# Kernel optimization log

Hardware: AMD Instinct MI355X
Metric: run time of the kernel (lower is better)

The kernel has to match this reference:

```python
import jax, jax.numpy as jnp
import numpy as np

H = 64  # hidden_size

def _lstm_layer(x, Wih, Whh, bih, bhh):
    # x: [B,T,I]; Wih: [4H,I]; Whh: [4H,H]; biases: [4H]
    # PyTorch gate order: i, f, g, o
    xg = jnp.einsum('bti,gi->btg', x, Wih) + (bih + bhh)  # [B,T,4H]
    B = x.shape[0]
    h0 = jnp.zeros((B, H), x.dtype)
    c0 = jnp.zeros((B, H), x.dtype)

    def step(carry, xg_t):
        h, c = carry
        gates = xg_t + h @ Whh.T  # [B,4H]
        i, f, g, o = jnp.split(gates, 4, axis=-1)
        i = jax.nn.sigmoid(i)
        f = jax.nn.sigmoid(f)
        g = jnp.tanh(g)
        o = jax.nn.sigmoid(o)
        c = f * c + i * g
        h = o * jnp.tanh(c)
        return (h, c), h

    _, hs = jax.lax.scan(step, (h0, c0), jnp.swapaxes(xg, 0, 1))  # hs: [T,B,H]
    return jnp.swapaxes(hs, 0, 1)  # [B,T,H]


def setup_inputs() -> dict:
    key = jax.random.key(0)
    ks = jax.random.split(key, 13)
    B, T, I = 1024, 512, 32
    s = 0.1
    return {
        'x': jax.random.normal(ks[0], (B, T, I), jnp.float32),
        'Wih0': jax.random.normal(ks[1], (4 * H, I), jnp.float32) * s,
        'Whh0': jax.random.normal(ks[2], (4 * H, H), jnp.float32) * s,
        'bih0': jax.random.normal(ks[3], (4 * H,), jnp.float32) * s,
        'bhh0': jax.random.normal(ks[4], (4 * H,), jnp.float32) * s,
        'Wih1': jax.random.normal(ks[5], (4 * H, H), jnp.float32) * s,
        'Whh1': jax.random.normal(ks[6], (4 * H, H), jnp.float32) * s,
        'bih1': jax.random.normal(ks[7], (4 * H,), jnp.float32) * s,
        'bhh1': jax.random.normal(ks[8], (4 * H,), jnp.float32) * s,
        'fc1_w': jax.random.normal(ks[9], (32, H), jnp.float32) * s,
        'fc1_b': jax.random.normal(ks[10], (32,), jnp.float32) * s,
        'fc2_w': jax.random.normal(ks[11], (2, 32), jnp.float32) * s,
        'fc2_b': jax.random.normal(ks[12], (2,), jnp.float32) * s,
    }


def reference(x, Wih0, Whh0, bih0, bhh0, Wih1, Whh1, bih1, bhh1, fc1_w, fc1_b, fc2_w, fc2_b):
    # Inference mode: dropout layers are identity.
    h1 = _lstm_layer(x, Wih0, Whh0, bih0, bhh0)   # [B,T,H]
    h2 = _lstm_layer(h1, Wih1, Whh1, bih1, bhh1)  # [B,T,H]
    h = h2[:, -1, :]                               # [B,H]
    z = jax.nn.relu(h @ fc1_w.T + fc1_b)           # [B,32]
    return z @ fc2_w.T + fc2_b                     # [B,2]
```

## Files before the change

### kernel.cpp

```cpp
#include <hip/hip_runtime.h>
#include <math.h>

#define TLEN 512
#define NB   1024
#define HSTR 80
#define HLAY (4 * HSTR)
#define XCH  64
#define XBSTR (XCH * 32 + 16)
#define XHALF (4 * XBSTR)

#define NLOG2E  (-1.44269504f)
#define N2LOG2E (-2.88539008f)

typedef _Float16 f16;
typedef f16   f16x4 __attribute__((ext_vector_type(4)));
typedef f16   f16x8 __attribute__((ext_vector_type(8)));
typedef float f32x4 __attribute__((ext_vector_type(4)));

__device__ __forceinline__ float ex2(float x) {
#if __has_builtin(__builtin_amdgcn_exp2f)
    return __builtin_amdgcn_exp2f(x);
#else
    return exp2f(x);
#endif
}
__device__ __forceinline__ float rcp_(float x) { return __builtin_amdgcn_rcpf(x); }
__device__ __forceinline__ float sel4(f32x4 v, int g) {
    float a = (g & 1) ? v[1] : v[0];
    float b = (g & 1) ? v[3] : v[2];
    return (g & 2) ? b : a;
}

__global__ __launch_bounds__(512, 2) void lstm_fused(
    const float* __restrict__ x,
    const float* __restrict__ Wih0, const float* __restrict__ Whh0,
    const float* __restrict__ bih0, const float* __restrict__ bhh0,
    const float* __restrict__ Wih1, const float* __restrict__ Whh1,
    const float* __restrict__ bih1, const float* __restrict__ bhh1,
    const float* __restrict__ fc1w, const float* __restrict__ fc1b,
    const float* __restrict__ fc2w, const float* __restrict__ fc2b,
    float* __restrict__ out)
{
    __shared__ __align__(16) f16 x_lds[2 * XHALF];
    __shared__ __align__(16) f16 h1buf[2 * HLAY];
    __shared__ __align__(16) f16 h2buf[2 * HLAY];
    __shared__ float zbuf[4][33];

    const int tid   = threadIdx.x;
    const int lane  = tid & 63;
    const int w     = tid >> 6;
    const int wg    = w & 3;
    const bool isL0 = (w < 4);
    const int bc    = lane & 15;
    const int lq    = lane >> 4;
    const int G     = bc >> 2;
    const int b_own = bc & 3;
    const int bg0   = blockIdx.x * 4;

    const float wsc[4] = {NLOG2E, NLOG2E, N2LOG2E, NLOG2E};
    f16x8 A[4][4];
    f32x4 cb[4];
    #pragma unroll
    for (int g = 0; g < 4; ++g) {
        const int gr = g * 64 + 16 * wg + bc;
        #pragma unroll
        for (int s = 0; s < 4; ++s) {
            #pragma unroll
            for (int i = 0; i < 8; ++i) {
                int k = 32 * s + lq * 8 + i;
                float v = 0.0f;
                if (isL0) {
                    if (s < 3) v = (k < 32) ? Wih0[gr * 32 + k] : Whh0[gr * 64 + (k - 32)];
                } else {
                    v = (k < 64) ? Wih1[gr * 64 + k] : Whh1[gr * 64 + (k - 64)];
                }
                A[g][s][i] = (f16)(v * wsc[g]);
            }
        }
        #pragma unroll
        for (int r = 0; r < 4; ++r) {
            const int gd = g * 64 + 16 * wg + 4 * lq + r;
            float bb = isL0 ? (bih0[gd] + bhh0[gd]) : (bih1[gd] + bhh1[gd]);
            cb[g][r] = bb * wsc[g];
        }
    }

    for (int i = tid; i < 2 * HLAY; i += 512) { h1buf[i] = (f16)0; h2buf[i] = (f16)0; }

    const int rf_b   = tid >> 7;
    const int rf_rem = tid & 127;
#define REFILL(ch)                                                            \
    {                                                                         \
        f16* dst = x_lds + ((ch) & 1) * XHALF + rf_b * XBSTR;                 \
        const float4* src = (const float4*)(x +                               \
            ((long)(bg0 + rf_b) * TLEN + (ch) * XCH) * 32);                   \
        float4 v0 = src[rf_rem];                                              \
        float4 v1 = src[rf_rem + 128];                                        \
        float4 v2 = src[rf_rem + 256];                                        \
        float4 v3 = src[rf_rem + 384];                                        \
        f16x4 h;                                                              \
        h[0]=(f16)v0.x; h[1]=(f16)v0.y; h[2]=(f16)v0.z; h[3]=(f16)v0.w;       \
        *(f16x4*)(dst + (rf_rem)       * 4) = h;                              \
        h[0]=(f16)v1.x; h[1]=(f16)v1.y; h[2]=(f16)v1.z; h[3]=(f16)v1.w;       \
        *(f16x4*)(dst + (rf_rem + 128) * 4) = h;                              \
        h[0]=(f16)v2.x; h[1]=(f16)v2.y; h[2]=(f16)v2.z; h[3]=(f16)v2.w;       \
        *(f16x4*)(dst + (rf_rem + 256) * 4) = h;                              \
        h[0]=(f16)v3.x; h[1]=(f16)v3.y; h[2]=(f16)v3.z; h[3]=(f16)v3.w;       \
        *(f16x4*)(dst + (rf_rem + 384) * 4) = h;                              \
    }

    REFILL(0)
    __syncthreads();

    const int bch = b_own * HSTR + lq * 8;
    const int bxx = b_own * XBSTR + lq * 8;
    const int hwr = b_own * HSTR + 16 * wg + 4 * lq + G;

    float cst = 0.0f;

#define CELL_UPDATE(HBUF, PW)                                                 \
    {                                                                         \
        float pi = sel4(a0, G);                                               \
        float pf = sel4(a1, G);                                               \
        float pg = sel4(a2, G);                                               \
        float po = sel4(a3, G);                                               \
        float iv = rcp_(1.0f + ex2(pi));                                      \
        float fv = rcp_(1.0f + ex2(pf));                                      \
        float gv = fmaf(2.0f, rcp_(1.0f + ex2(pg)), -1.0f);                   \
        float ov = rcp_(1.0f + ex2(po));                                      \
        cst = fmaf(fv, cst, iv * gv);                                         \
        float tc = fmaf(2.0f, rcp_(1.0f + ex2(cst * N2LOG2E)), -1.0f);        \
        HBUF[(PW) * HLAY + hwr] = (f16)(ov * tc);                             \
    }

#define L0_PHASE(p, itv)                                                      \
    {                                                                         \
        f16x8 b0 = *(const f16x8*)(x_lds + (((itv) >> 6) & 1) * XHALF +       \
                                   ((itv) & (XCH - 1)) * 32 + bxx);           \
        f16x8 b1 = *(const f16x8*)(h1buf + ((p)^1) * HLAY + bch);             \
        f16x8 b2 = *(const f16x8*)(h1buf + ((p)^1) * HLAY + bch + 32);        \
        __builtin_amdgcn_s_setprio(1);                                        \
        f32x4 a0 = __builtin_amdgcn_mfma_f32_16x16x32_f16(A[0][0], b0, cb[0], 0,0,0); \
        f32x4 a1 = __builtin_amdgcn_mfma_f32_16x16x32_f16(A[1][0], b0, cb[1], 0,0,0); \
        f32x4 a2 = __builtin_amdgcn_mfma_f32_16x16x32_f16(A[2][0], b0, cb[2], 0,0,0); \
        f32x4 a3 = __builtin_amdgcn_mfma_f32_16x16x32_f16(A[3][0], b0, cb[3], 0,0,0); \
        a0 = __builtin_amdgcn_mfma_f32_16x16x32_f16(A[0][1], b1, a0, 0,0,0);  \
        a1 = __builtin_amdgcn_mfma_f32_16x16x32_f16(A[1][1], b1, a1, 0,0,0);  \
        a2 = __builtin_amdgcn_mfma_f32_16x16x32_f16(A[2][1], b1, a2, 0,0,0);  \
        a3 = __builtin_amdgcn_mfma_f32_16x16x32_f16(A[3][1], b1, a3, 0,0,0);  \
        a0 = __builtin_amdgcn_mfma_f32_16x16x32_f16(A[0][2], b2, a0, 0,0,0);  \
        a1 = __builtin_amdgcn_mfma_f32_16x16x32_f16(A[1][2], b2, a1, 0,0,0);  \
        a2 = __builtin_amdgcn_mfma_f32_16x16x32_f16(A[2][2], b2, a2, 0,0,0);  \
        a3 = __builtin_amdgcn_mfma_f32_16x16x32_f16(A[3][2], b2, a3, 0,0,0);  \
        __builtin_amdgcn_s_setprio(0);                                        \
        CELL_UPDATE(h1buf, p)                                                 \
    }

#define L1_PHASE(p)                                                           \
    {                                                                         \
        f16x8 b0 = *(const f16x8*)(h1buf + ((p)^1) * HLAY + bch);             \
        f16x8 b1 = *(const f16x8*)(h1buf + ((p)^1) * HLAY + bch + 32);        \
        f16x8 b2 = *(const f16x8*)(h2buf + (p) * HLAY + bch);                 \
        f16x8 b3 = *(const f16x8*)(h2buf + (p) * HLAY + bch + 32);            \
        __builtin_amdgcn_s_setprio(1);                                        \
        f32x4 a0 = __builtin_amdgcn_mfma_f32_16x16x32_f16(A[0][0], b0, cb[0], 0,0,0); \
        f32x4 a1 = __builtin_amdgcn_mfma_f32_16x16x32_f16(A[1][0], b0, cb[1], 0,0,0); \
        f32x4 a2 = __builtin_amdgcn_mfma_f32_16x16x32_f16(A[2][0], b0, cb[2], 0,0,0); \
        f32x4 a3 = __builtin_amdgcn_mfma_f32_16x16x32_f16(A[3][0], b0, cb[3], 0,0,0); \
        a0 = __builtin_amdgcn_mfma_f32_16x16x32_f16(A[0][1], b1, a0, 0,0,0);  \
        a1 = __builtin_amdgcn_mfma_f32_16x16x32_f16(A[1][1], b1, a1, 0,0,0);  \
        a2 = __builtin_amdgcn_mfma_f32_16x16x32_f16(A[2][1], b1, a2, 0,0,0);  \
        a3 = __builtin_amdgcn_mfma_f32_16x16x32_f16(A[3][1], b1, a3, 0,0,0);  \
        a0 = __builtin_amdgcn_mfma_f32_16x16x32_f16(A[0][2], b2, a0, 0,0,0);  \
        a1 = __builtin_amdgcn_mfma_f32_16x16x32_f16(A[1][2], b2, a1, 0,0,0);  \
        a2 = __builtin_amdgcn_mfma_f32_16x16x32_f16(A[2][2], b2, a2, 0,0,0);  \
        a3 = __builtin_amdgcn_mfma_f32_16x16x32_f16(A[3][2], b2, a3, 0,0,0);  \
        a0 = __builtin_amdgcn_mfma_f32_16x16x32_f16(A[0][3], b3, a0, 0,0,0);  \
        a1 = __builtin_amdgcn_mfma_f32_16x16x32_f16(A[1][3], b3, a1, 0,0,0);  \
        a2 = __builtin_amdgcn_mfma_f32_16x16x32_f16(A[2][3], b3, a2, 0,0,0);  \
        a3 = __builtin_amdgcn_mfma_f32_16x16x32_f16(A[3][3], b3, a3, 0,0,0);  \
        __builtin_amdgcn_s_setprio(0);                                        \
        CELL_UPDATE(h2buf, (p)^1)                                             \
    }

    if (isL0) L0_PHASE(0, 0)
    REFILL(1)
    __syncthreads();

    #pragma unroll 1
    for (int k = 0; k < 255; ++k) {
        if (isL0) L0_PHASE(1, 2 * k + 1) else L1_PHASE(1)
        __syncthreads();
        const int it2 = 2 * k + 2;
        if (isL0) L0_PHASE(0, it2) else L1_PHASE(0)
        if ((it2 & (XCH - 1)) == 0 && it2 <= TLEN - 2 * XCH)
            REFILL((it2 >> 6) + 1)
        __syncthreads();
    }

    if (isL0) L0_PHASE(1, 511) else L1_PHASE(1)
    __syncthreads();
    if (!isL0) L1_PHASE(0)
    __syncthreads();

#undef L0_PHASE
#undef L1_PHASE
#undef CELL_UPDATE
#undef REFILL

    const f16* h2f = h2buf + HLAY;
    if (tid < 128) {
        int b = tid >> 5, m = tid & 31;
        float z = fc1b[m];
        #pragma unroll
        for (int j = 0; j < 64; ++j)
            z = fmaf(fc1w[m * 64 + j], (float)h2f[b * HSTR + j], z);
        zbuf[b][m] = fmaxf(z, 0.0f);
    }
    __syncthreads();
    if (tid < 8) {
        int b = tid >> 1, o = tid & 1;
        float s = fc2b[o];
        #pragma unroll
        for (int m = 0; m < 32; ++m)
            s = fmaf(fc2w[o * 32 + m], zbuf[b][m], s);
        out[(long)(bg0 + b) * 2 + o] = s;
    }
}

extern "C" void kernel_launch(void* const* d_in, const int* in_sizes, int n_in,
                              void* d_out, int out_size, void* d_ws, size_t ws_size,
                              hipStream_t stream) {
    const float* x    = (const float*)d_in[0];
    const float* Wih0 = (const float*)d_in[1];
    const float* Whh0 = (const float*)d_in[2];
    const float* bih0 = (const float*)d_in[3];
    const float* bhh0 = (const float*)d_in[4];
    const float* Wih1 = (const float*)d_in[5];
    const float* Whh1 = (const float*)d_in[6];
    const float* bih1 = (const float*)d_in[7];
    const float* bhh1 = (const float*)d_in[8];
    const float* fc1w = (const float*)d_in[9];
    const float* fc1b = (const float*)d_in[10];
    const float* fc2w = (const float*)d_in[11];
    const float* fc2b = (const float*)d_in[12];
    float* out = (float*)d_out;

    lstm_fused<<<dim3(NB / 4), dim3(512), 0, stream>>>(
        x, Wih0, Whh0, bih0, bhh0, Wih1, Whh1, bih1, bhh1,
        fc1w, fc1b, fc2w, fc2b, out);
}
```

Measured before the change: 227.4 us.

## Split LSTM steps into MFMA and activation halves staggered between layers

```diff
diff --git a/kernel.cpp b/kernel.cpp
--- a/kernel.cpp
+++ b/kernel.cpp
@@ -31,7 +31,7 @@
     return (g & 2) ? b : a;
 }
 
-__global__ __launch_bounds__(512, 2) void lstm_fused(
+__global__ __launch_bounds__(512, 1) void lstm_fused(
     const float* __restrict__ x,
     const float* __restrict__ Wih0, const float* __restrict__ Whh0,
     const float* __restrict__ bih0, const float* __restrict__ bhh0,
@@ -89,27 +89,34 @@
 
     const int rf_b   = tid >> 7;
     const int rf_rem = tid & 127;
-#define REFILL(ch)                                                            \
+#define REFILL512(ch)                                                         \
     {                                                                         \
         f16* dst = x_lds + ((ch) & 1) * XHALF + rf_b * XBSTR;                 \
         const float4* src = (const float4*)(x +                               \
             ((long)(bg0 + rf_b) * TLEN + (ch) * XCH) * 32);                   \
-        float4 v0 = src[rf_rem];                                              \
-        float4 v1 = src[rf_rem + 128];                                        \
-        float4 v2 = src[rf_rem + 256];                                        \
-        float4 v3 = src[rf_rem + 384];                                        \
-        f16x4 h;                                                              \
-        h[0]=(f16)v0.x; h[1]=(f16)v0.y; h[2]=(f16)v0.z; h[3]=(f16)v0.w;       \
-        *(f16x4*)(dst + (rf_rem)       * 4) = h;                              \
-        h[0]=(f16)v1.x; h[1]=(f16)v1.y; h[2]=(f16)v1.z; h[3]=(f16)v1.w;       \
-        *(f16x4*)(dst + (rf_rem + 128) * 4) = h;                              \
-        h[0]=(f16)v2.x; h[1]=(f16)v2.y; h[2]=(f16)v2.z; h[3]=(f16)v2.w;       \
-        *(f16x4*)(dst + (rf_rem + 256) * 4) = h;                              \
-        h[0]=(f16)v3.x; h[1]=(f16)v3.y; h[2]=(f16)v3.z; h[3]=(f16)v3.w;       \
-        *(f16x4*)(dst + (rf_rem + 384) * 4) = h;                              \
-    }
-
-    REFILL(0)
+        _Pragma("unroll")                                                     \
+        for (int j = 0; j < 4; ++j) {                                         \
+            float4 v = src[rf_rem + 128 * j];                                 \
+            f16x4 hv;                                                         \
+            hv[0]=(f16)v.x; hv[1]=(f16)v.y; hv[2]=(f16)v.z; hv[3]=(f16)v.w;   \
+            *(f16x4*)(dst + (rf_rem + 128 * j) * 4) = hv;                     \
+        }                                                                     \
+    }
+#define REFILL256(ch)                                                         \
+    {                                                                         \
+        f16* dst = x_lds + ((ch) & 1) * XHALF + wg * XBSTR;                   \
+        const float4* src = (const float4*)(x +                               \
+            ((long)(bg0 + wg) * TLEN + (ch) * XCH) * 32);                     \
+        _Pragma("unroll")                                                     \
+        for (int j = 0; j < 8; ++j) {                                         \
+            float4 v = src[lane + 64 * j];                                    \
+            f16x4 hv;                                                         \
+            hv[0]=(f16)v.x; hv[1]=(f16)v.y; hv[2]=(f16)v.z; hv[3]=(f16)v.w;   \
+            *(f16x4*)(dst + (lane + 64 * j) * 4) = hv;                        \
+        }                                                                     \
+    }
+
+    REFILL512(0)
     __syncthreads();
 
     const int bch = b_own * HSTR + lq * 8;
@@ -117,33 +124,19 @@
     const int hwr = b_own * HSTR + 16 * wg + 4 * lq + G;
 
     float cst = 0.0f;
-
-#define CELL_UPDATE(HBUF, PW)                                                 \
-    {                                                                         \
-        float pi = sel4(a0, G);                                               \
-        float pf = sel4(a1, G);                                               \
-        float pg = sel4(a2, G);                                               \
-        float po = sel4(a3, G);                                               \
-        float iv = rcp_(1.0f + ex2(pi));                                      \
-        float fv = rcp_(1.0f + ex2(pf));                                      \
-        float gv = fmaf(2.0f, rcp_(1.0f + ex2(pg)), -1.0f);                   \
-        float ov = rcp_(1.0f + ex2(po));                                      \
-        cst = fmaf(fv, cst, iv * gv);                                         \
-        float tc = fmaf(2.0f, rcp_(1.0f + ex2(cst * N2LOG2E)), -1.0f);        \
-        HBUF[(PW) * HLAY + hwr] = (f16)(ov * tc);                             \
-    }
-
-#define L0_PHASE(p, itv)                                                      \
+    f32x4 a0 = {0.f,0.f,0.f,0.f}, a1 = a0, a2 = a0, a3 = a0;
+
+#define L0_MFMA(P, itv)                                                       \
     {                                                                         \
         f16x8 b0 = *(const f16x8*)(x_lds + (((itv) >> 6) & 1) * XHALF +       \
-                                   ((itv) & (XCH - 1)) * 32 + bxx);           \
-        f16x8 b1 = *(const f16x8*)(h1buf + ((p)^1) * HLAY + bch);             \
-        f16x8 b2 = *(const f16x8*)(h1buf + ((p)^1) * HLAY + bch + 32);        \
+                                   ((itv) & 63) * 32 + bxx);                  \
+        f16x8 b1 = *(const f16x8*)(h1buf + ((P)^1) * HLAY + bch);             \
+        f16x8 b2 = *(const f16x8*)(h1buf + ((P)^1) * HLAY + bch + 32);        \
         __builtin_amdgcn_s_setprio(1);                                        \
-        f32x4 a0 = __builtin_amdgcn_mfma_f32_16x16x32_f16(A[0][0], b0, cb[0], 0,0,0); \
-        f32x4 a1 = __builtin_amdgcn_mfma_f32_16x16x32_f16(A[1][0], b0, cb[1], 0,0,0); \
-        f32x4 a2 = __builtin_amdgcn_mfma_f32_16x16x32_f16(A[2][0], b0, cb[2], 0,0,0); \
-        f32x4 a3 = __builtin_amdgcn_mfma_f32_16x16x32_f16(A[3][0], b0, cb[3], 0,0,0); \
+        a0 = __builtin_amdgcn_mfma_f32_16x16x32_f16(A[0][0], b0, cb[0], 0,0,0); \
+        a1 = __builtin_amdgcn_mfma_f32_16x16x32_f16(A[1][0], b0, cb[1], 0,0,0); \
+        a2 = __builtin_amdgcn_mfma_f32_16x16x32_f16(A[2][0], b0, cb[2], 0,0,0); \
+        a3 = __builtin_amdgcn_mfma_f32_16x16x32_f16(A[3][0], b0, cb[3], 0,0,0); \
         a0 = __builtin_amdgcn_mfma_f32_16x16x32_f16(A[0][1], b1, a0, 0,0,0);  \
         a1 = __builtin_amdgcn_mfma_f32_16x16x32_f16(A[1][1], b1, a1, 0,0,0);  \
         a2 = __builtin_amdgcn_mfma_f32_16x16x32_f16(A[2][1], b1, a2, 0,0,0);  \
@@ -153,20 +146,19 @@
         a2 = __builtin_amdgcn_mfma_f32_16x16x32_f16(A[2][2], b2, a2, 0,0,0);  \
         a3 = __builtin_amdgcn_mfma_f32_16x16x32_f16(A[3][2], b2, a3, 0,0,0);  \
         __builtin_amdgcn_s_setprio(0);                                        \
-        CELL_UPDATE(h1buf, p)                                                 \
-    }
-
-#define L1_PHASE(p)                                                           \
-    {                                                                         \
-        f16x8 b0 = *(const f16x8*)(h1buf + ((p)^1) * HLAY + bch);             \
-        f16x8 b1 = *(const f16x8*)(h1buf + ((p)^1) * HLAY + bch + 32);        \
-        f16x8 b2 = *(const f16x8*)(h2buf + (p) * HLAY + bch);                 \
-        f16x8 b3 = *(const f16x8*)(h2buf + (p) * HLAY + bch + 32);            \
+    }
+
+#define L1_MFMA(P)                                                            \
+    {                                                                         \
+        f16x8 b0 = *(const f16x8*)(h1buf + ((P)^1) * HLAY + bch);             \
+        f16x8 b1 = *(const f16x8*)(h1buf + ((P)^1) * HLAY + bch + 32);        \
+        f16x8 b2 = *(const f16x8*)(h2buf + (P) * HLAY + bch);                 \
+        f16x8 b3 = *(const f16x8*)(h2buf + (P) * HLAY + bch + 32);            \
         __builtin_amdgcn_s_setprio(1);                                        \
-        f32x4 a0 = __builtin_amdgcn_mfma_f32_16x16x32_f16(A[0][0], b0, cb[0], 0,0,0); \
-        f32x4 a1 = __builtin_amdgcn_mfma_f32_16x16x32_f16(A[1][0], b0, cb[1], 0,0,0); \
-        f32x4 a2 = __builtin_amdgcn_mfma_f32_16x16x32_f16(A[2][0], b0, cb[2], 0,0,0); \
-        f32x4 a3 = __builtin_amdgcn_mfma_f32_16x16x32_f16(A[3][0], b0, cb[3], 0,0,0); \
+        a0 = __builtin_amdgcn_mfma_f32_16x16x32_f16(A[0][0], b0, cb[0], 0,0,0); \
+        a1 = __builtin_amdgcn_mfma_f32_16x16x32_f16(A[1][0], b0, cb[1], 0,0,0); \
+        a2 = __builtin_amdgcn_mfma_f32_16x16x32_f16(A[2][0], b0, cb[2], 0,0,0); \
+        a3 = __builtin_amdgcn_mfma_f32_16x16x32_f16(A[3][0], b0, cb[3], 0,0,0); \
         a0 = __builtin_amdgcn_mfma_f32_16x16x32_f16(A[0][1], b1, a0, 0,0,0);  \
         a1 = __builtin_amdgcn_mfma_f32_16x16x32_f16(A[1][1], b1, a1, 0,0,0);  \
         a2 = __builtin_amdgcn_mfma_f32_16x16x32_f16(A[2][1], b1, a2, 0,0,0);  \
@@ -180,33 +172,61 @@
         a2 = __builtin_amdgcn_mfma_f32_16x16x32_f16(A[2][3], b3, a2, 0,0,0);  \
         a3 = __builtin_amdgcn_mfma_f32_16x16x32_f16(A[3][3], b3, a3, 0,0,0);  \
         __builtin_amdgcn_s_setprio(0);                                        \
-        CELL_UPDATE(h2buf, (p)^1)                                             \
-    }
-
-    if (isL0) L0_PHASE(0, 0)
-    REFILL(1)
+    }
+
+#define ACT_STORE(HBUF, P)                                                    \
+    {                                                                         \
+        float pi = sel4(a0, G);                                               \
+        float pf = sel4(a1, G);                                               \
+        float pg = sel4(a2, G);                                               \
+        float po = sel4(a3, G);                                               \
+        float iv = rcp_(1.0f + ex2(pi));                                      \
+        float fv = rcp_(1.0f + ex2(pf));                                      \
+        float gv = fmaf(2.0f, rcp_(1.0f + ex2(pg)), -1.0f);                   \
+        float ov = rcp_(1.0f + ex2(po));                                      \
+        cst = fmaf(fv, cst, iv * gv);                                         \
+        float tc = fmaf(2.0f, rcp_(1.0f + ex2(cst * N2LOG2E)), -1.0f);        \
+        HBUF[(P) * HLAY + hwr] = (f16)(ov * tc);                              \
+    }
+
+    if (isL0) { L0_MFMA(0, 0) } else { REFILL256(1) }
+    __syncthreads();
+    if (isL0) { ACT_STORE(h1buf, 0) }
+    __syncthreads();
+    if (isL0) { L0_MFMA(1, 1) }
+    __syncthreads();
+    if (isL0) { ACT_STORE(h1buf, 1) } else { L1_MFMA(1) }
     __syncthreads();
 
     #pragma unroll 1
-    for (int k = 0; k < 255; ++k) {
-        if (isL0) L0_PHASE(1, 2 * k + 1) else L1_PHASE(1)
-        __syncthreads();
-        const int it2 = 2 * k + 2;
-        if (isL0) L0_PHASE(0, it2) else L1_PHASE(0)
-        if ((it2 & (XCH - 1)) == 0 && it2 <= TLEN - 2 * XCH)
-            REFILL((it2 >> 6) + 1)
-        __syncthreads();
-    }
-
-    if (isL0) L0_PHASE(1, 511) else L1_PHASE(1)
-    __syncthreads();
-    if (!isL0) L1_PHASE(0)
-    __syncthreads();
-
-#undef L0_PHASE
-#undef L1_PHASE
-#undef CELL_UPDATE
-#undef REFILL
+    for (int k = 1; k <= 255; ++k) {
+        const int phe = 2 * k;
+        if (isL0) { L0_MFMA(0, phe) }
+        else {
+            ACT_STORE(h2buf, 0)
+            if ((phe & 63) == 0 && phe <= 384) REFILL256((phe >> 6) + 1)
+        }
+        __syncthreads();
+        if (isL0) { ACT_STORE(h1buf, 0) } else { L1_MFMA(0) }
+        __syncthreads();
+        if (isL0) { L0_MFMA(1, phe + 1) } else { ACT_STORE(h2buf, 1) }
+        __syncthreads();
+        if (isL0) { ACT_STORE(h1buf, 1) } else { L1_MFMA(1) }
+        __syncthreads();
+    }
+
+    if (!isL0) { ACT_STORE(h2buf, 0) }
+    __syncthreads();
+    if (!isL0) { L1_MFMA(0) }
+    __syncthreads();
+    if (!isL0) { ACT_STORE(h2buf, 1) }
+    __syncthreads();
+
+#undef L0_MFMA
+#undef L1_MFMA
+#undef ACT_STORE
+#undef REFILL512
+#undef REFILL256
 
     const f16* h2f = h2buf + HLAY;
     if (tid < 128) {
```

New measurement: 253.6 us. 11.5% more time.
